# Kernel tuning notes

Hardware: AMD Instinct MI355X
Metric: run time of the kernel (lower is better)

Reference implementation:

```python
import jax, jax.numpy as jnp
import numpy as np

B, T, IDIM = 16, 1024, 345
L, D, H, DK, FF = 4, 256, 4, 64, 1024
EPS = 1e-5


def layer_norm(x, s, b):
    m = jnp.mean(x, axis=-1, keepdims=True)
    v = jnp.mean(jnp.square(x - m), axis=-1, keepdims=True)
    return (x - m) * jax.lax.rsqrt(v + EPS) * s + b


def setup_inputs() -> dict:
    key = jax.random.key(0)
    ks = jax.random.split(key, 16)
    w = 0.02
    return {
        "x": jax.random.normal(ks[0], (B, T, IDIM), jnp.float32),
        "num_frames": int(T),
        "Win": w * jax.random.normal(ks[1], (IDIM, D), jnp.float32),
        "b_in": jnp.zeros((D,), jnp.float32),
        "ln1_s": jnp.ones((L, D), jnp.float32),
        "ln1_b": jnp.zeros((L, D), jnp.float32),
        "Wq": w * jax.random.normal(ks[2], (L, D, D), jnp.float32),
        "bq": jnp.zeros((L, D), jnp.float32),
        "Wk": w * jax.random.normal(ks[3], (L, D, D), jnp.float32),
        "bk": jnp.zeros((L, D), jnp.float32),
        "Wv": w * jax.random.normal(ks[4], (L, D, D), jnp.float32),
        "bv": jnp.zeros((L, D), jnp.float32),
        "Wo": w * jax.random.normal(ks[5], (L, D, D), jnp.float32),
        "bo": jnp.zeros((L, D), jnp.float32),
        "ln2_s": jnp.ones((L, D), jnp.float32),
        "ln2_b": jnp.zeros((L, D), jnp.float32),
        "W1": w * jax.random.normal(ks[6], (L, D, FF), jnp.float32),
        "b1": jnp.zeros((L, FF), jnp.float32),
        "W2": w * jax.random.normal(ks[7], (L, FF, D), jnp.float32),
        "b2": jnp.zeros((L, D), jnp.float32),
        "lno_s": jnp.ones((D,), jnp.float32),
        "lno_b": jnp.zeros((D,), jnp.float32),
    }


def reference(x, num_frames, Win, b_in, ln1_s, ln1_b, Wq, bq, Wk, bk, Wv, bv,
              Wo, bo, ln2_s, ln2_b, W1, b1, W2, b2, lno_s, lno_b):
    num = x.shape[0]
    scale = 1.0 / np.sqrt(DK)
    # [num*T, D]
    e = x.reshape(-1, x.shape[-1]) @ Win + b_in
    for i in range(L):
        e = layer_norm(e, ln1_s[i], ln1_b[i])
        # naive MHSA (residual taken from LN output, as in the source)
        q = (e @ Wq[i] + bq[i]).reshape(num, -1, H, DK)
        k = (e @ Wk[i] + bk[i]).reshape(num, -1, H, DK)
        v = (e @ Wv[i] + bv[i]).reshape(num, -1, H, DK)
        scores = jnp.einsum('bqhd,bkhd->bhqk', q, k) * scale
        attn = jax.nn.softmax(scores, axis=-1)
        o = jnp.einsum('bhqk,bkhd->bqhd', attn, v).reshape(-1, D)
        e = e + (o @ Wo[i] + bo[i])
        e = layer_norm(e, ln2_s[i], ln2_b[i])
        e = e + (jax.nn.relu(e @ W1[i] + b1[i]) @ W2[i] + b2[i])
    out = layer_norm(e, lno_s, lno_b)
    return out.reshape(num, num_frames, -1)
```

## Files before the change

### kernel.cpp

```cpp
#include <hip/hip_runtime.h>
#include <hip/hip_bf16.h>

#define BB    16
#define TT    1024
#define MTOK  (BB*TT)
#define IDIM_ 345
#define KPAD  384
#define LL    4
#define DD_   256
#define FF_   1024
#define EPS_  1e-5f
#define QSCL  0.18033688f

typedef __bf16 bf16;
typedef bf16 bf16x8 __attribute__((ext_vector_type(8)));
typedef float f32x4 __attribute__((ext_vector_type(4)));

static __device__ __forceinline__ f32x4 MFMA(bf16x8 a, bf16x8 b, f32x4 c) {
  return __builtin_amdgcn_mfma_f32_16x16x32_bf16(a, b, c, 0, 0, 0);
}
static __device__ __forceinline__ unsigned bfbits(float x) {
  return (unsigned)__builtin_bit_cast(unsigned short, (bf16)x);
}
static __device__ __forceinline__ bf16x8 ld_bf8(const void* p) {
  return *reinterpret_cast<const bf16x8*>(p);
}
static __device__ __forceinline__ void gload_lds16(const bf16* g, void* l) {
  __builtin_amdgcn_global_load_lds(
      (const __attribute__((address_space(1))) void*)g,
      (__attribute__((address_space(3))) void*)l, 16, 0, 0);
}

__global__ void k_convert_pad(const float* __restrict__ src, bf16* __restrict__ dst) {
  int idx = blockIdx.x * 256 + threadIdx.x;
  if (idx >= MTOK * (KPAD / 4)) return;
  int r = idx / (KPAD / 4), c0 = (idx % (KPAD / 4)) * 4;
  const float* s = src + (long)r * IDIM_ + c0;
  float v0 = (c0 + 0 < IDIM_) ? s[0] : 0.f;
  float v1 = (c0 + 1 < IDIM_) ? s[1] : 0.f;
  float v2 = (c0 + 2 < IDIM_) ? s[2] : 0.f;
  float v3 = (c0 + 3 < IDIM_) ? s[3] : 0.f;
  uint2 pk;
  pk.x = bfbits(v0) | (bfbits(v1) << 16);
  pk.y = bfbits(v2) | (bfbits(v3) << 16);
  *reinterpret_cast<uint2*>(dst + (long)r * KPAD + c0) = pk;
}

__global__ void k_wt_convert(const float* __restrict__ src, bf16* __restrict__ dst,
                             int K, int N, int Kp) {
  int idx = blockIdx.x * 256 + threadIdx.x;
  if (idx >= N * Kp) return;
  int n = idx / Kp, kk = idx % Kp;
  dst[idx] = (kk < K) ? (bf16)src[(long)kk * N + n] : (bf16)0.f;
}

__global__ __launch_bounds__(256)
void k_wt_all(const float* __restrict__ Wq, const float* __restrict__ Wk,
              const float* __restrict__ Wv, const float* __restrict__ Wo,
              const float* __restrict__ W1, const float* __restrict__ W2,
              bf16* __restrict__ Wqkvt, bf16* __restrict__ Wot,
              bf16* __restrict__ W1t, bf16* __restrict__ W2t) {
  __shared__ float tile[64][65];
  const int s = blockIdx.y, m = s >> 2, i = s & 3;
  const float* src; bf16* dst; int K, N;
  switch (m) {
    case 0: src = Wq + (long)i*65536;  dst = Wqkvt + (long)i*196608;          K=256;  N=256;  break;
    case 1: src = Wk + (long)i*65536;  dst = Wqkvt + (long)i*196608 + 65536;  K=256;  N=256;  break;
    case 2: src = Wv + (long)i*65536;  dst = Wqkvt + (long)i*196608 + 131072; K=256;  N=256;  break;
    case 3: src = Wo + (long)i*65536;  dst = Wot + (long)i*65536;             K=256;  N=256;  break;
    case 4: src = W1 + (long)i*262144; dst = W1t + (long)i*262144;            K=256;  N=1024; break;
    default:src = W2 + (long)i*262144; dst = W2t + (long)i*262144;            K=1024; N=256;  break;
  }
  const int tiles_n = N >> 6, ntiles = (K >> 6) * tiles_n;
  if (blockIdx.x >= ntiles) return;
  const int tk = blockIdx.x / tiles_n, tn = blockIdx.x % tiles_n;
  const int t = threadIdx.x, rq = t >> 6, cl = t & 63;
  #pragma unroll
  for (int i2 = 0; i2 < 16; i2++)
    tile[rq * 16 + i2][cl] = src[(long)(tk * 64 + rq * 16 + i2) * N + tn * 64 + cl];
  __syncthreads();
  #pragma unroll
  for (int i2 = 0; i2 < 16; i2++)
    dst[(long)(tn * 64 + rq * 16 + i2) * K + tk * 64 + cl] = (bf16)tile[cl][rq * 16 + i2];
}

__global__ void k_bias_concat(const float* __restrict__ bq, const float* __restrict__ bk,
                              const float* __restrict__ bv, float* __restrict__ bqkv) {
  int idx = blockIdx.x * 256 + threadIdx.x;
  if (idx >= LL * 768) return;
  int i = idx / 768, j = idx % 768;
  float v = (j < 256) ? bq[i*256 + j] : (j < 512 ? bk[i*256 + j - 256] : bv[i*256 + j - 512]);
  bqkv[idx] = v;
}

template<int EPI>
__global__ __launch_bounds__(512, 4)
void k_gemm_row(const bf16* __restrict__ A, const bf16* __restrict__ Wt,
                const float* __restrict__ bias, const bf16* __restrict__ resid,
                const float* __restrict__ lns, const float* __restrict__ lnb,
                void* __restrict__ out, int K) {
  __shared__ alignas(16) char As[4096];
  __shared__ alignas(16) char Bs[32768];
  __shared__ alignas(16) float redS[32][4];
  __shared__ alignas(16) float redQ[32][4];
  const int t = threadIdx.x, lane = t & 63, wid = t >> 6;
  const int wr = wid >> 2, wc = wid & 3;
  const int g = lane >> 4, c = lane & 15;
  int flat = blockIdx.x;
  flat = (flat & 7) * 64 + (flat >> 3);
  const int mbase = flat * 32;

  const int srow = t >> 3;
  const int slot = ((t & 7) ^ (srow & 7)) * 8;
  const bf16* ag = A  + (long)(mbase + srow) * K + slot;
  const bf16* bg = Wt + (long)srow * K + slot;
  const int swz = (c & 7) << 4;

  f32x4 acc[4] = {};

  const int nk = K >> 6;
  for (int kt = 0; kt < nk; ++kt) {
    const int k0 = kt * 64;
    __syncthreads();
    if (wid < 4) gload_lds16(ag + k0, As + wid * 1024);
    #pragma unroll
    for (int p = 0; p < 4; p++)
      gload_lds16(bg + (long)(p * 64) * K + k0, Bs + p * 8192 + wid * 1024);
    __syncthreads();

    bf16x8 af[2], bfr[4][2];
    #pragma unroll
    for (int ks = 0; ks < 2; ks++)
      af[ks] = ld_bf8(As + (wr * 16 + c) * 128 + ((ks * 64 + g * 16) ^ swz));
    #pragma unroll
    for (int ni = 0; ni < 4; ni++)
      #pragma unroll
      for (int ks = 0; ks < 2; ks++)
        bfr[ni][ks] = ld_bf8(Bs + (wc * 64 + ni * 16 + c) * 128 + ((ks * 64 + g * 16) ^ swz));
    __builtin_amdgcn_s_setprio(1);
    #pragma unroll
    for (int ni = 0; ni < 4; ni++)
      #pragma unroll
      for (int ks = 0; ks < 2; ks++)
        acc[ni] = MFMA(af[ks], bfr[ni][ks], acc[ni]);
    __builtin_amdgcn_s_setprio(0);
  }

  float v[4][4];
  float sP[4] = {0.f, 0.f, 0.f, 0.f}, qP[4] = {0.f, 0.f, 0.f, 0.f};
  #pragma unroll
  for (int ni = 0; ni < 4; ni++) {
    const int col = wc * 64 + ni * 16 + c;
    const float bb = bias[col];
    #pragma unroll
    for (int j = 0; j < 4; j++) {
      const int row = mbase + wr * 16 + g * 4 + j;
      float r = resid ? (float)resid[(long)row * 256 + col] : 0.f;
      float x = acc[ni][j] + bb + r;
      v[ni][j] = x;
      sP[j] += x;
      qP[j] += x * x;
    }
  }
  #pragma unroll
  for (int j = 0; j < 4; j++) {
    #pragma unroll
    for (int off = 1; off < 16; off <<= 1) {
      sP[j] += __shfl_xor(sP[j], off);
      qP[j] += __shfl_xor(qP[j], off);
    }
  }
  if (c == 0) {
    #pragma unroll
    for (int j = 0; j < 4; j++) {
      const int rb = wr * 16 + g * 4 + j;
      redS[rb][wc] = sP[j];
      redQ[rb][wc] = qP[j];
    }
  }
  __syncthreads();

  #pragma unroll
  for (int j = 0; j < 4; j++) {
    const int rb = wr * 16 + g * 4 + j;
    const float4 s4 = *reinterpret_cast<const float4*>(redS[rb]);
    const float4 q4 = *reinterpret_cast<const float4*>(redQ[rb]);
    const float mean = (s4.x + s4.y + s4.z + s4.w) * (1.f / 256.f);
    const float var = (q4.x + q4.y + q4.z + q4.w) * (1.f / 256.f) - mean * mean;
    const float rstd = rsqrtf(var + EPS_);
    const long row = mbase + wr * 16 + g * 4 + j;
    #pragma unroll
    for (int ni = 0; ni < 4; ni++) {
      const int col = wc * 64 + ni * 16 + c;
      const float y = (v[ni][j] - mean) * rstd * lns[col] + lnb[col];
      if constexpr (EPI == 0) {
        ((bf16*)out)[row * 256 + col] = (bf16)y;
      } else {
        ((float*)out)[row * 256 + col] = y;
      }
    }
  }
}

template<int EPI>
__global__ __launch_bounds__(256)
void k_gemm_big(const bf16* __restrict__ A, const bf16* __restrict__ Wt,
                const float* __restrict__ bias, void* __restrict__ out,
                bf16* __restrict__ vt, int N, int K) {
  __shared__ alignas(16) char As[16384];
  __shared__ alignas(16) char Bs[16384];
  const int t = threadIdx.x, lane = t & 63, wid = t >> 6;
  const int wr = wid >> 1, wc = wid & 1;
  const int g = lane >> 4, c = lane & 15;
  int flat = blockIdx.y * gridDim.x + blockIdx.x;
  const int cpx = (gridDim.x * gridDim.y) >> 3;
  flat = (flat & 7) * cpx + (flat >> 3);
  const int mbase = (flat / gridDim.x) * 128, nbase = (flat % gridDim.x) * 128;

  const int srow = t >> 3;
  const int skc = ((t & 7) ^ (srow & 7)) * 8;
  const bf16* ag = A  + (long)(mbase + srow) * K + skc;
  const bf16* bg = Wt + (long)(nbase + srow) * K + skc;
  const int swz = (c & 7) << 4;

  f32x4 acc[4][4] = {};

  const int nk = K >> 6;
  for (int kt = 0; kt < nk; ++kt) {
    const int k0 = kt * 64;
    __syncthreads();
    #pragma unroll
    for (int p = 0; p < 4; p++) {
      gload_lds16(ag + (long)p * 32 * K + k0, As + p * 4096 + wid * 1024);
      gload_lds16(bg + (long)p * 32 * K + k0, Bs + p * 4096 + wid * 1024);
    }
    __syncthreads();

    bf16x8 af[4][2], bfr[4][2];
    #pragma unroll
    for (int mi = 0; mi < 4; mi++)
      #pragma unroll
      for (int ks = 0; ks < 2; ks++)
        af[mi][ks] = ld_bf8(As + (wr * 64 + mi * 16 + c) * 128 + ((ks * 64 + g * 16) ^ swz));
    #pragma unroll
    for (int ni = 0; ni < 4; ni++)
      #pragma unroll
      for (int ks = 0; ks < 2; ks++)
        bfr[ni][ks] = ld_bf8(Bs + (wc * 64 + ni * 16 + c) * 128 + ((ks * 64 + g * 16) ^ swz));
    __builtin_amdgcn_s_setprio(1);
    #pragma unroll
    for (int mi = 0; mi < 4; mi++)
      #pragma unroll
      for (int ni = 0; ni < 4; ni++)
        #pragma unroll
        for (int ks = 0; ks < 2; ks++)
          acc[mi][ni] = MFMA(af[mi][ks], bfr[ni][ks], acc[mi][ni]);
    __builtin_amdgcn_s_setprio(0);
  }

  #pragma unroll
  for (int mi = 0; mi < 4; mi++) {
    #pragma unroll
    for (int ni = 0; ni < 4; ni++) {
      const int colg = nbase + wc * 64 + ni * 16 + c;
      const float bv = bias ? bias[colg] : 0.f;
      if constexpr (EPI == 3) {
        if (nbase < 512) {
          const float qs = (nbase < 256) ? QSCL : 1.0f;
          #pragma unroll
          for (int j = 0; j < 4; j++) {
            const int rowg = mbase + wr * 64 + mi * 16 + g * 4 + j;
            ((bf16*)out)[(long)rowg * N + colg] = (bf16)((acc[mi][ni][j] + bv) * qs);
          }
        } else {
          const int dfull = colg - 512, hh = dfull >> 6, d = dfull & 63;
          const int rowg0 = mbase + wr * 64 + mi * 16 + g * 4;
          uint2 st;
          st.x = bfbits(acc[mi][ni][0] + bv) | (bfbits(acc[mi][ni][1] + bv) << 16);
          st.y = bfbits(acc[mi][ni][2] + bv) | (bfbits(acc[mi][ni][3] + bv) << 16);
          *reinterpret_cast<uint2*>(vt + (long)(((rowg0 >> 10) << 2) + hh) * 65536
                                       + d * 1024 + (rowg0 & 1023)) = st;
        }
      } else {
        #pragma unroll
        for (int j = 0; j < 4; j++) {
          const int rowg = mbase + wr * 64 + mi * 16 + g * 4 + j;
          ((bf16*)out)[(long)rowg * N + colg] = (bf16)fmaxf(acc[mi][ni][j] + bv, 0.f);
        }
      }
    }
  }
}

__global__ __launch_bounds__(256)
void k_attn(const bf16* __restrict__ qkv, const bf16* __restrict__ vtg,
            bf16* __restrict__ o) {
  __shared__ alignas(16) char Ks[2][8192];
  __shared__ alignas(16) char Vs[2][8192];
  __shared__ alignas(16) char Ps[16384];
  const int t = threadIdx.x, lane = t & 63, w = t >> 6;
  const int g = lane >> 4, c = lane & 15;
  int flat = blockIdx.y * 8 + blockIdx.x;
  flat = (flat & 7) * 64 + (flat >> 3);
  const int bh = flat >> 3, qt = flat & 7;
  const int b = bh >> 2, h = bh & 3;
  const long tokbase = (long)b * TT;
  const int qA = qt * 128 + w * 16 + c;
  const int qB = qA + 64;

  bf16x8 qf0A = ld_bf8(qkv + (tokbase + qA) * 768 + h * 64 + g * 8);
  bf16x8 qf1A = ld_bf8(qkv + (tokbase + qA) * 768 + h * 64 + 32 + g * 8);
  bf16x8 qf0B = ld_bf8(qkv + (tokbase + qB) * 768 + h * 64 + g * 8);
  bf16x8 qf1B = ld_bf8(qkv + (tokbase + qB) * 768 + h * 64 + 32 + g * 8);

  const int sr = t >> 3;
  const int slot = (t & 7) ^ (sr & 7);
  const int swz_c = (c & 7) << 4;
  const bf16* kbase = qkv + 256 + h * 64 + slot * 8;
  const bf16* vbase = vtg + (long)bh * 65536 + slot * 8;
  char* pwA = Ps + w * 4096 + c * 128;
  char* pwB = pwA + 2048;

#define KSTAGE(bi, jt) do { \
    gload_lds16(kbase + (tokbase + (jt) * 64 + sr) * 768,      Ks[bi] + w * 1024); \
    gload_lds16(kbase + (tokbase + (jt) * 64 + sr + 32) * 768, Ks[bi] + 4096 + w * 1024); \
    gload_lds16(vbase + (long)sr * 1024 + (jt) * 64,           Vs[bi] + w * 1024); \
    gload_lds16(vbase + (long)(sr + 32) * 1024 + (jt) * 64,    Vs[bi] + 4096 + w * 1024); \
  } while (0)

  f32x4 oaccA[4] = {}, oaccB[4] = {};
  float mrunA = -1e30f, lrunA = 0.f, mrunB = -1e30f, lrunB = 0.f;

  KSTAGE(0, 0);
  int cur = 0;
  for (int jt = 0; jt < 16; ++jt) {
    if (jt + 1 < 16) {
      KSTAGE(cur ^ 1, jt + 1);
      asm volatile("s_waitcnt vmcnt(4)" ::: "memory");
    } else {
      asm volatile("s_waitcnt vmcnt(0)" ::: "memory");
    }
    __builtin_amdgcn_s_barrier();

    f32x4 saccA[4] = {}, saccB[4] = {};
    __builtin_amdgcn_s_setprio(1);
    #pragma unroll
    for (int ni = 0; ni < 4; ni++) {
      const char* krow = Ks[cur] + (ni * 16 + c) * 128;
      bf16x8 kf0 = ld_bf8(krow + ((g * 16) ^ swz_c));
      bf16x8 kf1 = ld_bf8(krow + ((64 + g * 16) ^ swz_c));
      saccA[ni] = MFMA(kf0, qf0A, saccA[ni]);
      saccB[ni] = MFMA(kf0, qf0B, saccB[ni]);
      saccA[ni] = MFMA(kf1, qf1A, saccA[ni]);
      saccB[ni] = MFMA(kf1, qf1B, saccB[ni]);
    }
    __builtin_amdgcn_s_setprio(0);

    float mA = -1e30f, mB = -1e30f;
    #pragma unroll
    for (int ni = 0; ni < 4; ni++)
      #pragma unroll
      for (int j = 0; j < 4; j++) {
        mA = fmaxf(mA, saccA[ni][j]);
        mB = fmaxf(mB, saccB[ni][j]);
      }
    mA = fmaxf(mA, __shfl_xor(mA, 16));
    mB = fmaxf(mB, __shfl_xor(mB, 16));
    mA = fmaxf(mA, __shfl_xor(mA, 32));
    mB = fmaxf(mB, __shfl_xor(mB, 32));

    if (!__all(mA <= mrunA + 11.5f)) {
      const float mn = fmaxf(mrunA, mA);
      const float al = __builtin_amdgcn_exp2f(mrunA - mn);
      mrunA = mn; lrunA *= al;
      #pragma unroll
      for (int nd = 0; nd < 4; nd++)
        #pragma unroll
        for (int j = 0; j < 4; j++) oaccA[nd][j] *= al;
    }
    if (!__all(mB <= mrunB + 11.5f)) {
      const float mn = fmaxf(mrunB, mB);
      const float al = __builtin_amdgcn_exp2f(mrunB - mn);
      mrunB = mn; lrunB *= al;
      #pragma unroll
      for (int nd = 0; nd < 4; nd++)
        #pragma unroll
        for (int j = 0; j < 4; j++) oaccB[nd][j] *= al;
    }

    float rsA = 0.f, rsB = 0.f;
    #pragma unroll
    for (int ni = 0; ni < 4; ni++) {
      float a0 = __builtin_amdgcn_exp2f(saccA[ni][0] - mrunA);
      float b0 = __builtin_amdgcn_exp2f(saccB[ni][0] - mrunB);
      float a1 = __builtin_amdgcn_exp2f(saccA[ni][1] - mrunA);
      float b1 = __builtin_amdgcn_exp2f(saccB[ni][1] - mrunB);
      float a2 = __builtin_amdgcn_exp2f(saccA[ni][2] - mrunA);
      float b2 = __builtin_amdgcn_exp2f(saccB[ni][2] - mrunB);
      float a3 = __builtin_amdgcn_exp2f(saccA[ni][3] - mrunA);
      float b3 = __builtin_amdgcn_exp2f(saccB[ni][3] - mrunB);
      rsA += (a0 + a1) + (a2 + a3);
      rsB += (b0 + b1) + (b2 + b3);
      uint2 qa, qb;
      qa.x = bfbits(a0) | (bfbits(a1) << 16);
      qa.y = bfbits(a2) | (bfbits(a3) << 16);
      qb.x = bfbits(b0) | (bfbits(b1) << 16);
      qb.y = bfbits(b2) | (bfbits(b3) << 16);
      *reinterpret_cast<uint2*>(pwA + ((ni * 32 + g * 8) ^ swz_c)) = qa;
      *reinterpret_cast<uint2*>(pwB + ((ni * 32 + g * 8) ^ swz_c)) = qb;
    }
    rsA += __shfl_xor(rsA, 16);
    rsB += __shfl_xor(rsB, 16);
    rsA += __shfl_xor(rsA, 32);
    rsB += __shfl_xor(rsB, 32);
    lrunA += rsA;
    lrunB += rsB;

    __builtin_amdgcn_s_setprio(1);
    #pragma unroll
    for (int kk = 0; kk < 2; kk++) {
      bf16x8 pfA = ld_bf8(pwA + ((kk * 64 + g * 16) ^ swz_c));
      bf16x8 pfB = ld_bf8(pwB + ((kk * 64 + g * 16) ^ swz_c));
      #pragma unroll
      for (int nd = 0; nd < 4; nd++) {
        bf16x8 vf = ld_bf8(Vs[cur] + (nd * 16 + c) * 128 + ((kk * 64 + g * 16) ^ swz_c));
        oaccA[nd] = MFMA(vf, pfA, oaccA[nd]);
        oaccB[nd] = MFMA(vf, pfB, oaccB[nd]);
      }
    }
    __builtin_amdgcn_s_setprio(0);
    __builtin_amdgcn_s_barrier();
    cur ^= 1;
  }
#undef KSTAGE

  const float invA = 1.f / lrunA, invB = 1.f / lrunB;
  bf16* orowA = o + (tokbase + qA) * 256 + h * 64 + g * 4;
  bf16* orowB = o + (tokbase + qB) * 256 + h * 64 + g * 4;
  #pragma unroll
  for (int nd = 0; nd < 4; nd++) {
    uint2 sa, sb;
    sa.x = bfbits(oaccA[nd][0] * invA) | (bfbits(oaccA[nd][1] * invA) << 16);
    sa.y = bfbits(oaccA[nd][2] * invA) | (bfbits(oaccA[nd][3] * invA) << 16);
    sb.x = bfbits(oaccB[nd][0] * invB) | (bfbits(oaccB[nd][1] * invB) << 16);
    sb.y = bfbits(oaccB[nd][2] * invB) | (bfbits(oaccB[nd][3] * invB) << 16);
    *reinterpret_cast<uint2*>(orowA + nd * 16) = sa;
    *reinterpret_cast<uint2*>(orowB + nd * 16) = sb;
  }
}

extern "C" void kernel_launch(void* const* d_in, const int* in_sizes, int n_in,
                              void* d_out, int out_size, void* d_ws, size_t ws_size,
                              hipStream_t stream) {
  const float* x     = (const float*)d_in[0];
  const float* Win   = (const float*)d_in[2];
  const float* b_in  = (const float*)d_in[3];
  const float* ln1_s = (const float*)d_in[4];
  const float* ln1_b = (const float*)d_in[5];
  const float* Wq    = (const float*)d_in[6];
  const float* bq    = (const float*)d_in[7];
  const float* Wk    = (const float*)d_in[8];
  const float* bk    = (const float*)d_in[9];
  const float* Wv    = (const float*)d_in[10];
  const float* bv    = (const float*)d_in[11];
  const float* Wo    = (const float*)d_in[12];
  const float* bo    = (const float*)d_in[13];
  const float* ln2_s = (const float*)d_in[14];
  const float* ln2_b = (const float*)d_in[15];
  const float* W1    = (const float*)d_in[16];
  const float* b1    = (const float*)d_in[17];
  const float* W2    = (const float*)d_in[18];
  const float* b2    = (const float*)d_in[19];
  const float* lno_s = (const float*)d_in[20];
  const float* lno_b = (const float*)d_in[21];
  float* out = (float*)d_out;

  char* ws = (char*)d_ws;
  size_t off = 0;
  auto alloc = [&](size_t bytes) -> void* {
    void* p = ws + off; off += (bytes + 255) & ~(size_t)255; return p;
  };
  bf16* e_bf  = (bf16*)alloc((size_t)MTOK * DD_ * 2);
  bf16* qkvb  = (bf16*)alloc((size_t)MTOK * 768 * 2);
  bf16* vtb   = (bf16*)alloc((size_t)MTOK * DD_ * 2);
  bf16* ob    = (bf16*)alloc((size_t)MTOK * DD_ * 2);
  bf16* hb    = (bf16*)alloc((size_t)MTOK * FF_ * 2);
  bf16* x_bf  = (bf16*)hb;
  bf16* Wint  = (bf16*)alloc((size_t)DD_ * KPAD * 2);
  bf16* Wqkvt = (bf16*)alloc((size_t)LL * 768 * DD_ * 2);
  bf16* Wot   = (bf16*)alloc((size_t)LL * DD_ * DD_ * 2);
  bf16* W1t   = (bf16*)alloc((size_t)LL * DD_ * FF_ * 2);
  bf16* W2t   = (bf16*)alloc((size_t)LL * FF_ * DD_ * 2);
  float* bqkv = (float*)alloc((size_t)LL * 768 * 4);

  dim3 blk(256);

  k_convert_pad<<<(MTOK * (KPAD / 4) + 255) / 256, 256, 0, stream>>>(x, x_bf);
  k_wt_convert<<<(DD_ * KPAD + 255) / 256, 256, 0, stream>>>(Win, Wint, IDIM_, DD_, KPAD);
  k_wt_all<<<dim3(64, 24), blk, 0, stream>>>(Wq, Wk, Wv, Wo, W1, W2, Wqkvt, Wot, W1t, W2t);
  k_bias_concat<<<(LL * 768 + 255) / 256, 256, 0, stream>>>(bq, bk, bv, bqkv);

  k_gemm_row<0><<<512, 512, 0, stream>>>(x_bf, Wint, b_in, nullptr,
                                         ln1_s, ln1_b, e_bf, KPAD);

  const long DDW = (long)DD_ * DD_;
  const long DFF = (long)DD_ * FF_;
  for (int i = 0; i < LL; i++) {
    k_gemm_big<3><<<dim3(6, 128), blk, 0, stream>>>(e_bf, Wqkvt + (long)i * 768 * DD_,
                                                    bqkv + i * 768, qkvb, vtb, 768, DD_);
    k_attn<<<dim3(8, 64), blk, 0, stream>>>(qkvb, vtb, ob);
    k_gemm_row<0><<<512, 512, 0, stream>>>(ob, Wot + i * DDW, bo + i * DD_, e_bf,
                                           ln2_s + i * DD_, ln2_b + i * DD_, e_bf, DD_);
    k_gemm_big<1><<<dim3(8, 128), blk, 0, stream>>>(e_bf, W1t + i * DFF, b1 + i * FF_,
                                                    hb, nullptr, FF_, DD_);
    if (i < LL - 1) {
      k_gemm_row<0><<<512, 512, 0, stream>>>(hb, W2t + i * DFF, b2 + i * DD_, e_bf,
                                             ln1_s + (i + 1) * DD_, ln1_b + (i + 1) * DD_,
                                             e_bf, FF_);
    } else {
      k_gemm_row<1><<<512, 512, 0, stream>>>(hb, W2t + i * DFF, b2 + i * DD_, e_bf,
                                             lno_s, lno_b, out, FF_);
    }
  }
}
```

Baseline: 445.6 us.

## Double-buffer LDS tiles in row GEMM to overlap global loads with MFMA

Splits the A and B shared-memory tiles in the row-wise GEMM-plus-LayerNorm kernel into two buffers. The next K-tile's global-to-LDS loads are issued before computing on the current tile, with an explicit vmcnt wait and raw barriers in place of __syncthreads. The goal is to hide global load latency behind the MFMA work. The cost is roughly double the LDS per block, which may cut the number of resident blocks per CU.

```diff
diff --git a/kernel.cpp b/kernel.cpp
--- a/kernel.cpp
+++ b/kernel.cpp
@@ -99,8 +99,8 @@
                 const float* __restrict__ bias, const bf16* __restrict__ resid,
                 const float* __restrict__ lns, const float* __restrict__ lnb,
                 void* __restrict__ out, int K) {
-  __shared__ alignas(16) char As[4096];
-  __shared__ alignas(16) char Bs[32768];
+  __shared__ alignas(16) char As[2][4096];
+  __shared__ alignas(16) char Bs[2][32768];
   __shared__ alignas(16) float redS[32][4];
   __shared__ alignas(16) float redQ[32][4];
   const int t = threadIdx.x, lane = t & 63, wid = t >> 6;
@@ -118,25 +118,34 @@
 
   f32x4 acc[4] = {};
 
+#define RSTAGE(bi, k0) do { \
+    if (wid < 4) gload_lds16(ag + (k0), As[bi] + wid * 1024); \
+    _Pragma("unroll") \
+    for (int p = 0; p < 4; p++) \
+      gload_lds16(bg + (long)(p * 64) * K + (k0), Bs[bi] + p * 8192 + wid * 1024); \
+  } while (0)
+
   const int nk = K >> 6;
+  RSTAGE(0, 0);
+  int cur = 0;
   for (int kt = 0; kt < nk; ++kt) {
-    const int k0 = kt * 64;
-    __syncthreads();
-    if (wid < 4) gload_lds16(ag + k0, As + wid * 1024);
-    #pragma unroll
-    for (int p = 0; p < 4; p++)
-      gload_lds16(bg + (long)(p * 64) * K + k0, Bs + p * 8192 + wid * 1024);
-    __syncthreads();
+    if (kt + 1 < nk) {
+      RSTAGE(cur ^ 1, (kt + 1) * 64);
+      asm volatile("s_waitcnt vmcnt(4)" ::: "memory");
+    } else {
+      asm volatile("s_waitcnt vmcnt(0)" ::: "memory");
+    }
+    __builtin_amdgcn_s_barrier();
 
     bf16x8 af[2], bfr[4][2];
     #pragma unroll
     for (int ks = 0; ks < 2; ks++)
-      af[ks] = ld_bf8(As + (wr * 16 + c) * 128 + ((ks * 64 + g * 16) ^ swz));
+      af[ks] = ld_bf8(As[cur] + (wr * 16 + c) * 128 + ((ks * 64 + g * 16) ^ swz));
     #pragma unroll
     for (int ni = 0; ni < 4; ni++)
       #pragma unroll
       for (int ks = 0; ks < 2; ks++)
-        bfr[ni][ks] = ld_bf8(Bs + (wc * 64 + ni * 16 + c) * 128 + ((ks * 64 + g * 16) ^ swz));
+        bfr[ni][ks] = ld_bf8(Bs[cur] + (wc * 64 + ni * 16 + c) * 128 + ((ks * 64 + g * 16) ^ swz));
     __builtin_amdgcn_s_setprio(1);
     #pragma unroll
     for (int ni = 0; ni < 4; ni++)
@@ -144,7 +153,10 @@
       for (int ks = 0; ks < 2; ks++)
         acc[ni] = MFMA(af[ks], bfr[ni][ks], acc[ni]);
     __builtin_amdgcn_s_setprio(0);
-  }
+    __builtin_amdgcn_s_barrier();
+    cur ^= 1;
+  }
+#undef RSTAGE
 
   float v[4][4];
   float sP[4] = {0.f, 0.f, 0.f, 0.f}, qP[4] = {0.f, 0.f, 0.f, 0.f};
```

After: 453.5 us. No clear change (+1.8%).
